# Kernel optimization log

Measured on AMD Instinct MI355X. Metric: run time of the kernel, lower is better.

The kernel has to match this reference:

```python
import jax, jax.numpy as jnp
import numpy as np

L, C, F, K = 8192, 2048, 128, 257  # timesteps, input_size, filter_size, lag (odd => symmetric 'same' pad)
NY = 256  # number of overwritten channel rows


def setup_inputs() -> dict:
    key = jax.random.key(0)
    k1, k2, k3, k4 = jax.random.split(key, 4)
    x = jax.random.normal(k1, (L, C), dtype=jnp.float32)
    Yt = jax.random.randint(k2, (NY,), 0, C)
    # learned parameters (torch.rand -> uniform[0,1))
    g = jax.random.uniform(k3, (C, F), dtype=jnp.float32)
    kernel = jax.random.uniform(k4, (F, K), dtype=jnp.float32)
    return {"x": x, "Yt": Yt, "g": g, "kernel": kernel}


def reference(x, Yt, g, kernel):
    # synapse[c] is the per-channel 1D filter; the original builds a dense
    # (C, C, K) kernel whose only non-zero slices are the diagonal, so the
    # full conv1d is mathematically a depthwise (grouped) conv.
    synapse = jnp.matmul(g, kernel)          # (C, K)
    lhs = x.T[None]                          # (1, C, L)  NCH
    rhs = synapse[:, None, :]                # (C, 1, K)  OIH, groups=C
    pad = (kernel.shape[1] - 1) // 2         # torch padding='same', odd K
    out = jax.lax.conv_general_dilated(
        lhs, rhs,
        window_strides=(1,),
        padding=[(pad, pad)],
        feature_group_count=x.shape[1],
        dimension_numbers=("NCH", "OIH", "NCH"),
    )                                        # (1, C, L)
    # result[:, Yt, :] = x.T[Yt] : scatter-overwrite selected channel rows
    out = out.at[:, Yt, :].set(x.T[Yt][None])
    return out
```

## Files before the change

### kernel.cpp

```cpp
#include <hip/hip_runtime.h>

#define LL   8192
#define CC   2048
#define FF   128
#define KK   257
#define PAD  128

#define XROW 8448
#define SROW 320
#define NT   18

typedef __bf16 bf16x8 __attribute__((ext_vector_type(8)));
typedef float  f32x16 __attribute__((ext_vector_type(16)));

static __device__ __forceinline__ unsigned short f2bf(float f) {
    unsigned u = __float_as_uint(f);
    u = (u + 0x7fffu + ((u >> 16) & 1u)) >> 16;
    return (unsigned short)u;
}


__global__ __launch_bounds__(256) void synb_kernel(const float* __restrict__ g,
                                                   const float* __restrict__ kern,
                                                   const int* __restrict__ Yt, int ny,
                                                   unsigned short* __restrict__ synEb) {
    __shared__ int sfl[4];
    const int c0 = blockIdx.x * 4;
    const int t  = threadIdx.x;
    if (t < 4) sfl[t] = 0;
    __syncthreads();
    for (int i = t; i < ny; i += 256) {
        int y = Yt[i];
        #pragma unroll
        for (int ii = 0; ii < 4; ++ii) if (y == c0 + ii) sfl[ii] = 1;
    }
    __syncthreads();
    const float* g0 = g + (size_t)(c0 + 0) * FF;
    const float* g1 = g + (size_t)(c0 + 1) * FF;
    const float* g2 = g + (size_t)(c0 + 2) * FF;
    const float* g3 = g + (size_t)(c0 + 3) * FF;
    const int fl0 = sfl[0], fl1 = sfl[1], fl2 = sfl[2], fl3 = sfl[3];
    for (int p = t; p < SROW; p += 256) {
        const int kk = p - 32;
        float a0 = 0.f, a1 = 0.f, a2 = 0.f, a3 = 0.f;
        const bool inr = (kk >= 0) && (kk < KK);
        if (inr) {
            #pragma unroll 8
            for (int f = 0; f < FF; ++f) {
                float kv = kern[f * KK + kk];
                a0 += kv * g0[f];
                a1 += kv * g1[f];
                a2 += kv * g2[f];
                a3 += kv * g3[f];
            }
        }
        float dlt = (kk == PAD) ? 1.f : 0.f;
        float v0 = inr ? (fl0 ? dlt : a0) : 0.f;
        float v1 = inr ? (fl1 ? dlt : a1) : 0.f;
        float v2 = inr ? (fl2 ? dlt : a2) : 0.f;
        float v3 = inr ? (fl3 ? dlt : a3) : 0.f;
        synEb[(size_t)(c0 + 0) * SROW + p] = f2bf(v0);
        synEb[(size_t)(c0 + 1) * SROW + p] = f2bf(v1);
        synEb[(size_t)(c0 + 2) * SROW + p] = f2bf(v2);
        synEb[(size_t)(c0 + 3) * SROW + p] = f2bf(v3);
    }
}

__global__ __launch_bounds__(256) void xpose_kernel(const float* __restrict__ x,
                                                    unsigned short* __restrict__ xbp) {
    __shared__ float tile[64][65];
    const int l0 = blockIdx.x << 6;
    const int c0 = blockIdx.y << 6;
    const int t  = threadIdx.x;
    const int cl = t & 63, ls = t >> 6;
    #pragma unroll
    for (int k = 0; k < 16; ++k) {
        int ll = (k << 2) + ls;
        tile[ll][cl] = x[(size_t)(l0 + ll) * CC + c0 + cl];
    }
    __syncthreads();
    const int l2 = (t & 31) << 1, cg = t >> 5;
    #pragma unroll
    for (int k = 0; k < 8; ++k) {
        int cc = (k << 3) + cg;
        ushort2 v;
        v.x = f2bf(tile[l2 + 0][cc]);
        v.y = f2bf(tile[l2 + 1][cc]);
        *(ushort2*)(xbp + (size_t)(c0 + cc) * XROW + PAD + l0 + l2) = v;
    }
    if (blockIdx.x == 0) {
        for (int k = 0; k < 32; ++k) {
            int idx = (k << 8) + t, ch = idx >> 7, p = idx & 127;
            xbp[(size_t)(c0 + ch) * XROW + p] = 0;
        }
    } else if (blockIdx.x == 127) {
        for (int k = 0; k < 32; ++k) {
            int idx = (k << 8) + t, ch = idx >> 7, p = idx & 127;
            xbp[(size_t)(c0 + ch) * XROW + PAD + LL + p] = 0;
        }
    }
}

__global__ __launch_bounds__(256, 3) void conv_mfma(const unsigned short* __restrict__ xbp,
                                                    const unsigned short* __restrict__ synEb,
                                                    float* __restrict__ out) {
    __shared__ int4 xw[2][4][192];
    __shared__ unsigned short synL[4][SROW];
    const int w  = threadIdx.x >> 6;
    const int ln = threadIdx.x & 63;
    const int c  = (blockIdx.x << 2) + w;
    const int j  = ln & 31;
    const int q  = ln >> 5;

    {
        const unsigned short* srow = synEb + (size_t)c * SROW;
        #pragma unroll
        for (int k = 0; k < 5; ++k) synL[w][ln + 64 * k] = srow[ln + 64 * k];
    }

    const unsigned short* xrow = xbp + (size_t)c * XROW;
    int4 st0, st1, st2;
    {
        const int4* src = (const int4*)xrow;
        st0 = src[ln];
        st1 = src[ln + 64];
        if (ln < 32) st2 = src[ln + 128];
        int g0 = ln,      s0 = g0 ^ ((g0 >> 3) & 7);
        int g1 = ln + 64, s1 = g1 ^ ((g1 >> 3) & 7);
        xw[0][w][s0] = st0;
        xw[0][w][s1] = st1;
        if (ln < 32) { int g2 = ln + 128, s2 = g2 ^ ((g2 >> 3) & 7); xw[0][w][s2] = st2; }
    }
    __syncthreads();

    bf16x8 bfrag[NT];
    #pragma unroll
    for (int m = 0; m < NT; ++m) {
        union { unsigned short u[8]; bf16x8 v; } B;
        #pragma unroll
        for (int r = 0; r < 8; ++r)
            B.u[r] = synL[w][16 * m + 8 * q + r - j + 32];
        bfrag[m] = B.v;
    }

    const int gb = 4 * j + q;
    float* orow = out + (size_t)c * (size_t)LL + j;

    for (int lt = 0; lt < 8; ++lt) {
        const int buf = lt & 1;
        if (lt < 7) {
            const int4* src = (const int4*)(xrow + ((lt + 1) << 10));
            st0 = src[ln];
            st1 = src[ln + 64];
            if (ln < 32) st2 = src[ln + 128];
        }
        f32x16 acc;
        #pragma unroll
        for (int r = 0; r < 16; ++r) acc[r] = 0.0f;
        #pragma unroll
        for (int m = 0; m < NT; ++m) {
            int gm = gb + 2 * m;
            union { int4 i4; bf16x8 v; } A;
            A.i4 = xw[buf][w][gm ^ ((gm >> 3) & 7)];
            acc = __builtin_amdgcn_mfma_f32_32x32x16_bf16(A.v, bfrag[m], acc, 0, 0, 0);
        }
        float* o = orow + (lt << 10);
        #pragma unroll
        for (int r = 0; r < 16; ++r) {
            int row = (r & 3) + ((r >> 2) << 3) + (q << 2);
            o[row << 5] = acc[r];
        }
        if (lt < 7) {
            int g0 = ln,      s0 = g0 ^ ((g0 >> 3) & 7);
            int g1 = ln + 64, s1 = g1 ^ ((g1 >> 3) & 7);
            xw[buf ^ 1][w][s0] = st0;
            xw[buf ^ 1][w][s1] = st1;
            if (ln < 32) { int g2 = ln + 128, s2 = g2 ^ ((g2 >> 3) & 7); xw[buf ^ 1][w][s2] = st2; }
        }
        __syncthreads();
    }
}

#define KP 260
#define TL 32

__global__ void flag_kernel(const int* __restrict__ Yt, int ny, int* __restrict__ flag) {
    int t = threadIdx.x;
    for (int i = t; i < CC; i += blockDim.x) flag[i] = 0;
    __syncthreads();
    for (int i = t; i < ny; i += blockDim.x) flag[Yt[i]] = 1;
}

__global__ __launch_bounds__(256) void syn_kernel(const float* __restrict__ g,
                                                  const float* __restrict__ kern,
                                                  const int* __restrict__ flag,
                                                  float* __restrict__ synP) {
    const int c0 = blockIdx.x * 4;
    const int tid = threadIdx.x;
    const float* g0 = g + (size_t)(c0 + 0) * FF;
    const float* g1 = g + (size_t)(c0 + 1) * FF;
    const float* g2 = g + (size_t)(c0 + 2) * FF;
    const float* g3 = g + (size_t)(c0 + 3) * FF;
    const int fl0 = flag[c0 + 0], fl1 = flag[c0 + 1];
    const int fl2 = flag[c0 + 2], fl3 = flag[c0 + 3];
    for (int kk = tid; kk < KK; kk += 256) {
        float a0 = 0.f, a1 = 0.f, a2 = 0.f, a3 = 0.f;
        #pragma unroll 8
        for (int f = 0; f < FF; ++f) {
            float kv = kern[f * KK + kk];
            a0 += kv * g0[f]; a1 += kv * g1[f]; a2 += kv * g2[f]; a3 += kv * g3[f];
        }
        float dlt = (kk == PAD) ? 1.f : 0.f;
        synP[(size_t)(c0 + 0) * KP + kk] = fl0 ? dlt : a0;
        synP[(size_t)(c0 + 1) * KP + kk] = fl1 ? dlt : a1;
        synP[(size_t)(c0 + 2) * KP + kk] = fl2 ? dlt : a2;
        synP[(size_t)(c0 + 3) * KP + kk] = fl3 ? dlt : a3;
    }
}

template<bool EDGE>
__device__ __forceinline__ void conv_body(const float* __restrict__ xcol,
                                          const float* __restrict__ srow,
                                          float (&acc)[TL], int lbase) {
    float W[TL + 16];
    #pragma unroll
    for (int jj = 0; jj < TL + 16; ++jj) {
        int idx = lbase + jj;
        float v = 0.f;
        if (!EDGE || (unsigned)idx < (unsigned)LL) v = xcol[(size_t)idx * CC];
        W[jj] = v;
    }
    for (int s = 0; s < 16; ++s) {
        if (s) {
            #pragma unroll
            for (int jj = 0; jj < TL; ++jj) W[jj] = W[jj + 16];
            #pragma unroll
            for (int jj = 0; jj < 16; ++jj) {
                int idx = lbase + 16 * s + TL + jj;
                float v = 0.f;
                if (!EDGE || (unsigned)idx < (unsigned)LL) v = xcol[(size_t)idx * CC];
                W[TL + jj] = v;
            }
        }
        #pragma unroll
        for (int qq = 0; qq < 4; ++qq) {
            float4 sq = *(const float4*)(srow + 16 * s + 4 * qq);
            #pragma unroll
            for (int jj = 0; jj < TL; ++jj) acc[jj] += W[4 * qq + 0 + jj] * sq.x;
            #pragma unroll
            for (int jj = 0; jj < TL; ++jj) acc[jj] += W[4 * qq + 1 + jj] * sq.y;
            #pragma unroll
            for (int jj = 0; jj < TL; ++jj) acc[jj] += W[4 * qq + 2 + jj] * sq.z;
            #pragma unroll
            for (int jj = 0; jj < TL; ++jj) acc[jj] += W[4 * qq + 3 + jj] * sq.w;
        }
    }
    float s256 = srow[256];
    #pragma unroll
    for (int jj = 0; jj < TL; ++jj) acc[jj] += W[16 + jj] * s256;
}

__global__ __launch_bounds__(256) void conv_kernel(const float* __restrict__ x,
                                                   const float* __restrict__ synP,
                                                   float* __restrict__ out) {
    const int c  = blockIdx.y * blockDim.x + threadIdx.x;
    const int l0 = blockIdx.x * TL;
    const int lbase = l0 - PAD;
    const float* xcol = x + c;
    const float* srow = synP + (size_t)c * KP;
    float acc[TL];
    #pragma unroll
    for (int jj = 0; jj < TL; ++jj) acc[jj] = 0.f;
    const bool interior = (l0 >= PAD) && (l0 + TL + PAD <= LL);
    if (interior) conv_body<false>(xcol, srow, acc, lbase);
    else          conv_body<true>(xcol, srow, acc, lbase);
    float4* o = (float4*)(out + (size_t)c * LL + l0);
    #pragma unroll
    for (int qq = 0; qq < TL / 4; ++qq)
        o[qq] = make_float4(acc[4 * qq + 0], acc[4 * qq + 1], acc[4 * qq + 2], acc[4 * qq + 3]);
}

extern "C" void kernel_launch(void* const* d_in, const int* in_sizes, int n_in,
                              void* d_out, int out_size, void* d_ws, size_t ws_size,
                              hipStream_t stream) {
    const float* x    = (const float*)d_in[0];
    const int*   Yt   = (const int*)  d_in[1];
    const float* g    = (const float*)d_in[2];
    const float* kern = (const float*)d_in[3];
    float* out = (float*)d_out;
    const int ny = in_sizes[1];

    const size_t xbp_bytes = (size_t)CC * XROW * sizeof(unsigned short);
    const size_t syn_bytes = (size_t)CC * SROW * sizeof(unsigned short);

    if (ws_size >= xbp_bytes + syn_bytes) {
        unsigned short* xbp   = (unsigned short*)d_ws;
        unsigned short* synEb = (unsigned short*)((char*)d_ws + xbp_bytes);
        synb_kernel<<<CC / 4, 256, 0, stream>>>(g, kern, Yt, ny, synEb);
        xpose_kernel<<<dim3(LL / 64, CC / 64), 256, 0, stream>>>(x, xbp);
        conv_mfma<<<CC / 4, 256, 0, stream>>>(xbp, synEb, out);
    } else {
        float* synP = (float*)d_ws;
        int*   flag = (int*)((char*)d_ws + (size_t)CC * KP * sizeof(float));
        flag_kernel<<<1, 256, 0, stream>>>(Yt, ny, flag);
        syn_kernel<<<CC / 4, 256, 0, stream>>>(g, kern, flag, synP);
        conv_kernel<<<dim3(LL / TL, CC / 256), 256, 0, stream>>>(x, synP, out);
    }
}
```

Measured before the change: 149.9 us.

## Split conv along time into two blocks, drop barriers, widen transpose stores

The MFMA conv grid gains a second dimension that splits each channel's 8192 timesteps into two halves of four 1024-step tiles. This doubles the block count so more waves are resident per CU. Block-wide __syncthreads calls are removed, since each wave only touches its own LDS slices. The transpose kernel now writes four bf16 values per store instead of two, and the fp32 fallback path is deleted. The risk is that the code now relies on in-order LDS access within a wave, and that it assumes the workspace is always large enough.

```diff
diff --git a/kernel.cpp b/kernel.cpp
--- a/kernel.cpp
+++ b/kernel.cpp
@@ -9,6 +9,8 @@
 #define XROW 8448
 #define SROW 320
 #define NT   18
+#define SPLIT 2
+#define TILES 4
 
 typedef __bf16 bf16x8 __attribute__((ext_vector_type(8)));
 typedef float  f32x16 __attribute__((ext_vector_type(16)));
@@ -18,7 +20,6 @@
     u = (u + 0x7fffu + ((u >> 16) & 1u)) >> 16;
     return (unsigned short)u;
 }
-
 
 __global__ __launch_bounds__(256) void synb_kernel(const float* __restrict__ g,
                                                    const float* __restrict__ kern,
@@ -79,14 +80,16 @@
         tile[ll][cl] = x[(size_t)(l0 + ll) * CC + c0 + cl];
     }
     __syncthreads();
-    const int l2 = (t & 31) << 1, cg = t >> 5;
+    const int lw = (t & 15) << 2, cg = t >> 4;
     #pragma unroll
-    for (int k = 0; k < 8; ++k) {
-        int cc = (k << 3) + cg;
-        ushort2 v;
-        v.x = f2bf(tile[l2 + 0][cc]);
-        v.y = f2bf(tile[l2 + 1][cc]);
-        *(ushort2*)(xbp + (size_t)(c0 + cc) * XROW + PAD + l0 + l2) = v;
+    for (int k = 0; k < 4; ++k) {
+        int cc = (k << 4) + cg;
+        ushort4 v;
+        v.x = f2bf(tile[lw + 0][cc]);
+        v.y = f2bf(tile[lw + 1][cc]);
+        v.z = f2bf(tile[lw + 2][cc]);
+        v.w = f2bf(tile[lw + 3][cc]);
+        *(ushort4*)(xbp + (size_t)(c0 + cc) * XROW + PAD + l0 + lw) = v;
     }
     if (blockIdx.x == 0) {
         for (int k = 0; k < 32; ++k) {
@@ -108,7 +111,8 @@
     __shared__ unsigned short synL[4][SROW];
     const int w  = threadIdx.x >> 6;
     const int ln = threadIdx.x & 63;
-    const int c  = (blockIdx.x << 2) + w;
+    const int sp = blockIdx.x;
+    const int c  = (blockIdx.y << 2) + w;
     const int j  = ln & 31;
     const int q  = ln >> 5;
 
@@ -118,7 +122,7 @@
         for (int k = 0; k < 5; ++k) synL[w][ln + 64 * k] = srow[ln + 64 * k];
     }
 
-    const unsigned short* xrow = xbp + (size_t)c * XROW;
+    const unsigned short* xrow = xbp + (size_t)c * XROW + (size_t)(sp << 12);
     int4 st0, st1, st2;
     {
         const int4* src = (const int4*)xrow;
@@ -131,7 +135,6 @@
         xw[0][w][s1] = st1;
         if (ln < 32) { int g2 = ln + 128, s2 = g2 ^ ((g2 >> 3) & 7); xw[0][w][s2] = st2; }
     }
-    __syncthreads();
 
     bf16x8 bfrag[NT];
     #pragma unroll
@@ -144,11 +147,11 @@
     }
 
     const int gb = 4 * j + q;
-    float* orow = out + (size_t)c * (size_t)LL + j;
-
-    for (int lt = 0; lt < 8; ++lt) {
+    float* orow = out + (size_t)c * (size_t)LL + (sp << 12) + j;
+
+    for (int lt = 0; lt < TILES; ++lt) {
         const int buf = lt & 1;
-        if (lt < 7) {
+        if (lt < TILES - 1) {
             const int4* src = (const int4*)(xrow + ((lt + 1) << 10));
             st0 = src[ln];
             st1 = src[ln + 64];
@@ -170,114 +173,14 @@
             int row = (r & 3) + ((r >> 2) << 3) + (q << 2);
             o[row << 5] = acc[r];
         }
-        if (lt < 7) {
+        if (lt < TILES - 1) {
             int g0 = ln,      s0 = g0 ^ ((g0 >> 3) & 7);
             int g1 = ln + 64, s1 = g1 ^ ((g1 >> 3) & 7);
             xw[buf ^ 1][w][s0] = st0;
             xw[buf ^ 1][w][s1] = st1;
             if (ln < 32) { int g2 = ln + 128, s2 = g2 ^ ((g2 >> 3) & 7); xw[buf ^ 1][w][s2] = st2; }
         }
-        __syncthreads();
-    }
-}
-
-#define KP 260
-#define TL 32
-
-__global__ void flag_kernel(const int* __restrict__ Yt, int ny, int* __restrict__ flag) {
-    int t = threadIdx.x;
-    for (int i = t; i < CC; i += blockDim.x) flag[i] = 0;
-    __syncthreads();
-    for (int i = t; i < ny; i += blockDim.x) flag[Yt[i]] = 1;
-}
-
-__global__ __launch_bounds__(256) void syn_kernel(const float* __restrict__ g,
-                                                  const float* __restrict__ kern,
-                                                  const int* __restrict__ flag,
-                                                  float* __restrict__ synP) {
-    const int c0 = blockIdx.x * 4;
-    const int tid = threadIdx.x;
-    const float* g0 = g + (size_t)(c0 + 0) * FF;
-    const float* g1 = g + (size_t)(c0 + 1) * FF;
-    const float* g2 = g + (size_t)(c0 + 2) * FF;
-    const float* g3 = g + (size_t)(c0 + 3) * FF;
-    const int fl0 = flag[c0 + 0], fl1 = flag[c0 + 1];
-    const int fl2 = flag[c0 + 2], fl3 = flag[c0 + 3];
-    for (int kk = tid; kk < KK; kk += 256) {
-        float a0 = 0.f, a1 = 0.f, a2 = 0.f, a3 = 0.f;
-        #pragma unroll 8
-        for (int f = 0; f < FF; ++f) {
-            float kv = kern[f * KK + kk];
-            a0 += kv * g0[f]; a1 += kv * g1[f]; a2 += kv * g2[f]; a3 += kv * g3[f];
-        }
-        float dlt = (kk == PAD) ? 1.f : 0.f;
-        synP[(size_t)(c0 + 0) * KP + kk] = fl0 ? dlt : a0;
-        synP[(size_t)(c0 + 1) * KP + kk] = fl1 ? dlt : a1;
-        synP[(size_t)(c0 + 2) * KP + kk] = fl2 ? dlt : a2;
-        synP[(size_t)(c0 + 3) * KP + kk] = fl3 ? dlt : a3;
-    }
-}
-
-template<bool EDGE>
-__device__ __forceinline__ void conv_body(const float* __restrict__ xcol,
-                                          const float* __restrict__ srow,
-                                          float (&acc)[TL], int lbase) {
-    float W[TL + 16];
-    #pragma unroll
-    for (int jj = 0; jj < TL + 16; ++jj) {
-        int idx = lbase + jj;
-        float v = 0.f;
-        if (!EDGE || (unsigned)idx < (unsigned)LL) v = xcol[(size_t)idx * CC];
-        W[jj] = v;
-    }
-    for (int s = 0; s < 16; ++s) {
-        if (s) {
-            #pragma unroll
-            for (int jj = 0; jj < TL; ++jj) W[jj] = W[jj + 16];
-            #pragma unroll
-            for (int jj = 0; jj < 16; ++jj) {
-                int idx = lbase + 16 * s + TL + jj;
-                float v = 0.f;
-                if (!EDGE || (unsigned)idx < (unsigned)LL) v = xcol[(size_t)idx * CC];
-                W[TL + jj] = v;
-            }
-        }
-        #pragma unroll
-        for (int qq = 0; qq < 4; ++qq) {
-            float4 sq = *(const float4*)(srow + 16 * s + 4 * qq);
-            #pragma unroll
-            for (int jj = 0; jj < TL; ++jj) acc[jj] += W[4 * qq + 0 + jj] * sq.x;
-            #pragma unroll
-            for (int jj = 0; jj < TL; ++jj) acc[jj] += W[4 * qq + 1 + jj] * sq.y;
-            #pragma unroll
-            for (int jj = 0; jj < TL; ++jj) acc[jj] += W[4 * qq + 2 + jj] * sq.z;
-            #pragma unroll
-            for (int jj = 0; jj < TL; ++jj) acc[jj] += W[4 * qq + 3 + jj] * sq.w;
-        }
-    }
-    float s256 = srow[256];
-    #pragma unroll
-    for (int jj = 0; jj < TL; ++jj) acc[jj] += W[16 + jj] * s256;
-}
-
-__global__ __launch_bounds__(256) void conv_kernel(const float* __restrict__ x,
-                                                   const float* __restrict__ synP,
-                                                   float* __restrict__ out) {
-    const int c  = blockIdx.y * blockDim.x + threadIdx.x;
-    const int l0 = blockIdx.x * TL;
-    const int lbase = l0 - PAD;
-    const float* xcol = x + c;
-    const float* srow = synP + (size_t)c * KP;
-    float acc[TL];
-    #pragma unroll
-    for (int jj = 0; jj < TL; ++jj) acc[jj] = 0.f;
-    const bool interior = (l0 >= PAD) && (l0 + TL + PAD <= LL);
-    if (interior) conv_body<false>(xcol, srow, acc, lbase);
-    else          conv_body<true>(xcol, srow, acc, lbase);
-    float4* o = (float4*)(out + (size_t)c * LL + l0);
-    #pragma unroll
-    for (int qq = 0; qq < TL / 4; ++qq)
-        o[qq] = make_float4(acc[4 * qq + 0], acc[4 * qq + 1], acc[4 * qq + 2], acc[4 * qq + 3]);
+    }
 }
 
 extern "C" void kernel_launch(void* const* d_in, const int* in_sizes, int n_in,
@@ -291,19 +194,10 @@
     const int ny = in_sizes[1];
 
     const size_t xbp_bytes = (size_t)CC * XROW * sizeof(unsigned short);
-    const size_t syn_bytes = (size_t)CC * SROW * sizeof(unsigned short);
-
-    if (ws_size >= xbp_bytes + syn_bytes) {
-        unsigned short* xbp   = (unsigned short*)d_ws;
-        unsigned short* synEb = (unsigned short*)((char*)d_ws + xbp_bytes);
-        synb_kernel<<<CC / 4, 256, 0, stream>>>(g, kern, Yt, ny, synEb);
-        xpose_kernel<<<dim3(LL / 64, CC / 64), 256, 0, stream>>>(x, xbp);
-        conv_mfma<<<CC / 4, 256, 0, stream>>>(xbp, synEb, out);
-    } else {
-        float* synP = (float*)d_ws;
-        int*   flag = (int*)((char*)d_ws + (size_t)CC * KP * sizeof(float));
-        flag_kernel<<<1, 256, 0, stream>>>(Yt, ny, flag);
-        syn_kernel<<<CC / 4, 256, 0, stream>>>(g, kern, flag, synP);
-        conv_kernel<<<dim3(LL / TL, CC / 256), 256, 0, stream>>>(x, synP, out);
-    }
-}
+    unsigned short* xbp   = (unsigned short*)d_ws;
+    unsigned short* synEb = (unsigned short*)((char*)d_ws + xbp_bytes);
+
+    synb_kernel<<<CC / 4, 256, 0, stream>>>(g, kern, Yt, ny, synEb);
+    xpose_kernel<<<dim3(LL / 64, CC / 64), 256, 0, stream>>>(x, xbp);
+    conv_mfma<<<dim3(SPLIT, CC / 4), 256, 0, stream>>>(xbp, synEb, out);
+}
```

Result: no change. 152.2 us (+1.5%).
